# Kernel optimization log

Measured on AMD Instinct MI355X. Metric: run time of the kernel, lower is better.

The kernel has to match this reference:

```python
import jax, jax.numpy as jnp
import numpy as np

N = 640   # nodes
H = 64    # hidden_channels == base feature dim (required by MLP input dims)
DEG = 12  # random directed edges per node before symmetrization


def _mlp(x, Wa, ba, Wb, bb):
    # 2-layer MLP: Linear -> ReLU -> Linear (use_bn=False hardcoded in convs; dropout inactive in eval)
    return jax.nn.relu(x @ Wa + ba) @ Wb + bb


def setup_inputs() -> dict:
    key = jax.random.key(0)
    ks = jax.random.split(key, 8)
    x = jax.random.normal(ks[0], (N, H), dtype=jnp.float32)
    E0 = N * DEG
    src = jax.random.randint(ks[1], (E0,), 0, N)
    dst = jax.random.randint(ks[2], (E0,), 0, N)
    # undirected edge list (both directions), matching PyG k_hop_subgraph semantics on symmetric graphs
    edge_index = jnp.stack([jnp.concatenate([src, dst]), jnp.concatenate([dst, src])])
    batch = jnp.zeros((N,), dtype=jnp.int32)  # unused by the module's forward

    def lin(k, fin, fout):
        kw, kb = jax.random.split(k)
        bound = 1.0 / np.sqrt(fin)
        W = jax.random.uniform(kw, (fin, fout), minval=-bound, maxval=bound, dtype=jnp.float32)
        b = jax.random.uniform(kb, (fout,), minval=-bound, maxval=bound, dtype=jnp.float32)
        return W, b

    W1a, b1a = lin(ks[3], H + 2, H)      # convs[1] mlp: (H+t) -> H
    W1b, b1b = lin(ks[4], H, H + 1)      #               H -> (H+t-1)
    W0a, b0a = lin(ks[5], H + 1, H)      # convs[0] mlp: (H+1) -> H
    W0b, b0b = lin(ks[6], H, H)          #               H -> H
    return dict(x=x, W1a=W1a, b1a=b1a, W1b=W1b, b1b=b1b,
                W0a=W0a, b0a=b0a, W0b=W0b, b0b=b0b,
                edge_index=edge_index, batch=batch)


def reference(x, W1a, b1a, W1b, b1b, W0a, b0a, W0b, b0b, edge_index, batch):
    n = x.shape[0]
    # dense adjacency; self-loops have no effect in the original recursion -> zero diagonal
    A = jnp.zeros((n, n), x.dtype).at[edge_index[0], edge_index[1]].set(1.0)
    A = A * (1.0 - jnp.eye(n, dtype=x.dtype))

    # ---- level 1 (last level, r[1]=1), vectorized over all ego pairs (v, u) ----
    # S2(v,u) = nbrs(u) & S_v (common neighbors of v and u, excluding v, u)
    # sum_{w in S2} x_w  and  |S2|
    Y = A[:, :, None] * x[None, :, :]              # [v, w, d]
    T = jnp.einsum('vwd,uw->vud', Y, A)            # [v, u, d] = sum_w A[v,w] A[u,w] x_w
    cnt = A @ A.T                                  # [v, u] common-neighbor counts
    # hv_u = [x_u, 1, 0]; sum over S2 of [x_w, 1, 1]  ->  GIN input [x_u + T, 1 + cnt, cnt]
    inp1 = jnp.concatenate([x[None, :, :] + T,
                            (1.0 + cnt)[..., None],
                            cnt[..., None]], axis=-1)  # [v, u, H+2]
    out1 = _mlp(inp1, W1a, b1a, W1b, b1b)              # [v, u, H+1]

    # ---- level 0 (r[0]=1): GIN over u in S_v ----
    agg = jnp.einsum('vu,vud->vd', A, out1)            # sum of level-1 embeddings over S_v
    hv = jnp.concatenate([x, jnp.zeros((n, 1), x.dtype)], axis=-1)  # [x_v, 0]
    return _mlp(hv + agg, W0a, b0a, W0b, b0b)          # [N, H]
```

## Files before the change

kernel.cpp:

```cpp
#include <hip/hip_runtime.h>

#define NN   640
#define NW   20
#define NWP  24
#define H    64
#define MAXD 96

__global__ __launch_bounds__(512) void prep(
    const int* __restrict__ ei, int E,
    const float* __restrict__ x,
    const float* __restrict__ W1a, const float* __restrict__ W0a,
    const float* __restrict__ W1b, const float* __restrict__ b1b,
    unsigned* __restrict__ bits, float* __restrict__ xa, float* __restrict__ xc,
    float* __restrict__ Wf, float* __restrict__ bf)
{
    const int t = threadIdx.x, lane = t & 63, wave = t >> 6, bid = blockIdx.x;

    if (bid < 160) {
        __shared__ unsigned sb[4 * NW];
        if (t < 4 * NW) sb[t] = 0u;
        __syncthreads();

        const int quads = E >> 2;
        for (int k = t; k < quads; k += 512) {
            const int4 a4 = ((const int4*)ei)[k];
            if ((a4.x >> 2) == bid || (a4.y >> 2) == bid ||
                (a4.z >> 2) == bid || (a4.w >> 2) == bid) {
                const int4 b4 = ((const int4*)(ei + E))[k];
                if ((a4.x >> 2) == bid && a4.x != b4.x)
                    atomicOr(&sb[(a4.x & 3) * NW + (b4.x >> 5)], 1u << (b4.x & 31));
                if ((a4.y >> 2) == bid && a4.y != b4.y)
                    atomicOr(&sb[(a4.y & 3) * NW + (b4.y >> 5)], 1u << (b4.y & 31));
                if ((a4.z >> 2) == bid && a4.z != b4.z)
                    atomicOr(&sb[(a4.z & 3) * NW + (b4.z >> 5)], 1u << (b4.z & 31));
                if ((a4.w >> 2) == bid && a4.w != b4.w)
                    atomicOr(&sb[(a4.w & 3) * NW + (b4.w >> 5)], 1u << (b4.w & 31));
            }
        }
        for (int k = (quads << 2) + t; k < E; k += 512) {
            const int a = ei[k], b = ei[k + E];
            if ((a >> 2) == bid && a != b)
                atomicOr(&sb[(a & 3) * NW + (b >> 5)], 1u << (b & 31));
        }

        const int v = bid * 4 + (wave >> 1);
        const float* W = (wave & 1) ? W0a : W1a;
        const float xv = x[v * H + lane];
        float a0 = 0, a1 = 0, a2 = 0, a3 = 0;
        #pragma unroll
        for (int k = 0; k < H; k += 4) {
            a0 += __shfl(xv, k, 64)     * W[k * H + lane];
            a1 += __shfl(xv, k + 1, 64) * W[(k + 1) * H + lane];
            a2 += __shfl(xv, k + 2, 64) * W[(k + 2) * H + lane];
            a3 += __shfl(xv, k + 3, 64) * W[(k + 3) * H + lane];
        }
        float r = (a0 + a1) + (a2 + a3);
        if (wave & 1) xc[v * H + lane] = r; else xa[v * H + lane] = r;

        __syncthreads();
        if (t < 4 * NW) bits[(bid * 4 + t / NW) * NWP + (t % NW)] = sb[t];
    } else if (bid < 168) {
        const int d = (bid - 160) * 8 + wave;
        const float wv = W1b[d * 65 + lane];
        float a0 = 0, a1 = 0, a2 = 0, a3 = 0;
        #pragma unroll
        for (int e = 0; e < 64; e += 4) {
            a0 += __shfl(wv, e, 64)     * W0a[e * H + lane];
            a1 += __shfl(wv, e + 1, 64) * W0a[(e + 1) * H + lane];
            a2 += __shfl(wv, e + 2, 64) * W0a[(e + 2) * H + lane];
            a3 += __shfl(wv, e + 3, 64) * W0a[(e + 3) * H + lane];
        }
        Wf[d * H + lane] = (a0 + a1) + (a2 + a3) + W1b[d * 65 + 64] * W0a[64 * H + lane];
    } else if (wave == 0) {
        const float bv = b1b[lane];
        float a0 = 0, a1 = 0, a2 = 0, a3 = 0;
        #pragma unroll
        for (int e = 0; e < 64; e += 4) {
            a0 += __shfl(bv, e, 64)     * W0a[e * H + lane];
            a1 += __shfl(bv, e + 1, 64) * W0a[(e + 1) * H + lane];
            a2 += __shfl(bv, e + 2, 64) * W0a[(e + 2) * H + lane];
            a3 += __shfl(bv, e + 3, 64) * W0a[(e + 3) * H + lane];
        }
        bf[lane] = (a0 + a1) + (a2 + a3) + b1b[64] * W0a[64 * H + lane];
    }
}

__global__ __launch_bounds__(512, 6) void fused(
    const float* __restrict__ xa,  const float* __restrict__ xc,
    const float* __restrict__ W1a, const float* __restrict__ b1a,
    const float* __restrict__ Wf,  const float* __restrict__ bf,
    const float* __restrict__ b0a,
    const float* __restrict__ W0b, const float* __restrict__ b0b,
    const unsigned* __restrict__ bits,
    float* __restrict__ out)
{
    __shared__ __align__(16) unsigned rowv[NW];
    __shared__ __align__(16) unsigned nbs[MAXD * NW];
    __shared__ float xr[MAXD][H];
    __shared__ float p1[8][H];
    __shared__ float p2[8][H];
    __shared__ unsigned short ulist[MAXD];
    __shared__ int pre[NW];
    __shared__ int s_deg;

    const int v = blockIdx.x, t = threadIdx.x;
    const int lane = t & 63, wave = t >> 6;

    if (t < NW) rowv[t] = bits[v * NWP + t];
    __syncthreads();

    if (wave == 0) {
        unsigned word = (lane < NW) ? rowv[lane] : 0u;
        int pc = __popc(word), scan = pc;
        #pragma unroll
        for (int off = 1; off < 32; off <<= 1) {
            int nb = __shfl_up(scan, off, 64);
            if (lane >= off) scan += nb;
        }
        int o = scan - pc;
        if (lane < NW) pre[lane] = o;
        unsigned c = word;
        while (c) {
            int b = __ffs(c) - 1; c &= c - 1;
            if (o < MAXD) ulist[o] = (unsigned short)(lane * 32 + b);
            ++o;
        }
        if (lane == NW - 1) s_deg = (o < MAXD) ? o : MAXD;
    }
    __syncthreads();
    const int deg = s_deg;

    for (int p = wave; p < deg; p += 8)
        xr[p][lane] = xa[ulist[p] * H + lane];
    for (int idx = t; idx < deg * NW; idx += 512) {
        const int p = idx / NW, w = idx - p * NW;
        nbs[p * NW + w] = bits[ulist[p] * NWP + w];
    }

    const float r64 = W1a[64 * H + lane];
    const float k0  = b1a[lane] + r64;
    const float k1  = r64 + W1a[65 * H + lane];

    unsigned rw[NW];
    #pragma unroll
    for (int j = 0; j < NW; ++j) rw[j] = rowv[j];
    __syncthreads();

    float hacc = 0.f;
    for (int p = wave; p < deg; p += 8) {
        const uint4* bu = (const uint4*)(nbs + p * NW);
        const uint4 q0 = bu[0], q1 = bu[1], q2 = bu[2], q3 = bu[3], q4 = bu[4];
        unsigned cw[NW] = {
            rw[0]  & q0.x, rw[1]  & q0.y, rw[2]  & q0.z, rw[3]  & q0.w,
            rw[4]  & q1.x, rw[5]  & q1.y, rw[6]  & q1.z, rw[7]  & q1.w,
            rw[8]  & q2.x, rw[9]  & q2.y, rw[10] & q2.z, rw[11] & q2.w,
            rw[12] & q3.x, rw[13] & q3.y, rw[14] & q3.z, rw[15] & q3.w,
            rw[16] & q4.x, rw[17] & q4.y, rw[18] & q4.z, rw[19] & q4.w };
        int cnt = 0;
        #pragma unroll
        for (int j = 0; j < NW; ++j) cnt += __popc(cw[j]);
        float xs = 0.f;
        #pragma unroll
        for (int j = 0; j < NW; ++j) {
            unsigned c = cw[j];
            while (c) {
                int b = __ffs(c) - 1; c &= c - 1;
                int pos = pre[j] + __popc(rw[j] & ((1u << b) - 1));
                xs += xr[pos][lane];
            }
        }
        float h = xr[p][lane] + xs + k0 + (float)cnt * k1;
        hacc += fmaxf(h, 0.f);
    }
    p1[wave][lane] = hacc;
    __syncthreads();

    float hs = 0.f;
    #pragma unroll
    for (int w = 0; w < 8; ++w) hs += p1[w][lane];
    float s = 0.f;
    #pragma unroll
    for (int i = 0; i < 8; ++i) {
        const int d = wave * 8 + i;
        s += __shfl(hs, d, 64) * Wf[d * H + lane];
    }
    p2[wave][lane] = s;
    __syncthreads();

    float s2 = 0.f;
    #pragma unroll
    for (int w = 0; w < 8; ++w) s2 += p2[w][lane];
    const float hh = fmaxf(xc[v * H + lane] + (float)deg * bf[lane]
                           + b0a[lane] + s2, 0.f);
    float o = 0.f;
    #pragma unroll
    for (int i = 0; i < 8; ++i) {
        const int d = wave * 8 + i;
        o += __shfl(hh, d, 64) * W0b[d * H + lane];
    }
    p1[wave][lane] = o;
    __syncthreads();
    if (wave == 0) {
        float oo = b0b[lane];
        #pragma unroll
        for (int w = 0; w < 8; ++w) oo += p1[w][lane];
        out[v * H + lane] = oo;
    }
}

extern "C" void kernel_launch(void* const* d_in, const int* in_sizes, int n_in,
                              void* d_out, int out_size, void* d_ws, size_t ws_size,
                              hipStream_t stream) {
    const float* x   = (const float*)d_in[0];
    const float* W1a = (const float*)d_in[1];
    const float* b1a = (const float*)d_in[2];
    const float* W1b = (const float*)d_in[3];
    const float* b1b = (const float*)d_in[4];
    const float* W0a = (const float*)d_in[5];
    const float* b0a = (const float*)d_in[6];
    const float* W0b = (const float*)d_in[7];
    const float* b0b = (const float*)d_in[8];
    const int*   ei  = (const int*)d_in[9];
    const int    E   = in_sizes[9] / 2;

    char* ws = (char*)d_ws;
    unsigned* bits = (unsigned*)(ws);
    float*    xa   = (float*)(ws + 61440);
    float*    xc   = (float*)(ws + 61440 + 163840);
    float*    Wf   = (float*)(ws + 61440 + 2 * 163840);
    float*    bf   = (float*)(ws + 61440 + 2 * 163840 + 16384);

    prep<<<169, 512, 0, stream>>>(ei, E, x, W1a, W0a, W1b, b1b, bits, xa, xc, Wf, bf);
    fused<<<NN, 512, 0, stream>>>(xa, xc, W1a, b1a, Wf, bf, b0a, W0b, b0b,
                                  bits, (float*)d_out);
}
```

Baseline: 20.77 us.

## Compute neighbor list per wave in registers and batch edge loads in prep

In the fused kernel, each wave now reads the row bitmask straight into registers, computes prefix counts and walks the neighbor bits itself. Each wave gathers only the neighbor rows whose position maps to it. This removes the shared-memory ulist/pre/deg stage and two block-wide barriers, at the cost of every wave repeating the scalar bit walk. In prep, the edge-list scan preloads up to 8 int4 pairs per thread before doing the atomics, which gives more memory-level parallelism. It drops the early filter that skipped loading destinations, so more bytes are read.

New measurement: 23.95 us. 1.15x slower.

```diff
diff --git a/kernel.cpp b/kernel.cpp
--- a/kernel.cpp
+++ b/kernel.cpp
@@ -22,20 +22,40 @@
         __syncthreads();
 
         const int quads = E >> 2;
-        for (int k = t; k < quads; k += 512) {
+        int4 A[8], B[8];
+        #pragma unroll
+        for (int i = 0; i < 8; ++i) {
+            const int k = t + (i << 9);
+            if (k < quads) {
+                A[i] = ((const int4*)ei)[k];
+                B[i] = ((const int4*)(ei + E))[k];
+            }
+        }
+        #pragma unroll
+        for (int i = 0; i < 8; ++i) {
+            const int k = t + (i << 9);
+            if (k < quads) {
+                if ((A[i].x >> 2) == bid && A[i].x != B[i].x)
+                    atomicOr(&sb[(A[i].x & 3) * NW + (B[i].x >> 5)], 1u << (B[i].x & 31));
+                if ((A[i].y >> 2) == bid && A[i].y != B[i].y)
+                    atomicOr(&sb[(A[i].y & 3) * NW + (B[i].y >> 5)], 1u << (B[i].y & 31));
+                if ((A[i].z >> 2) == bid && A[i].z != B[i].z)
+                    atomicOr(&sb[(A[i].z & 3) * NW + (B[i].z >> 5)], 1u << (B[i].z & 31));
+                if ((A[i].w >> 2) == bid && A[i].w != B[i].w)
+                    atomicOr(&sb[(A[i].w & 3) * NW + (B[i].w >> 5)], 1u << (B[i].w & 31));
+            }
+        }
+        for (int k = t + (8 << 9); k < quads; k += 512) {
             const int4 a4 = ((const int4*)ei)[k];
-            if ((a4.x >> 2) == bid || (a4.y >> 2) == bid ||
-                (a4.z >> 2) == bid || (a4.w >> 2) == bid) {
-                const int4 b4 = ((const int4*)(ei + E))[k];
-                if ((a4.x >> 2) == bid && a4.x != b4.x)
-                    atomicOr(&sb[(a4.x & 3) * NW + (b4.x >> 5)], 1u << (b4.x & 31));
-                if ((a4.y >> 2) == bid && a4.y != b4.y)
-                    atomicOr(&sb[(a4.y & 3) * NW + (b4.y >> 5)], 1u << (b4.y & 31));
-                if ((a4.z >> 2) == bid && a4.z != b4.z)
-                    atomicOr(&sb[(a4.z & 3) * NW + (b4.z >> 5)], 1u << (b4.z & 31));
-                if ((a4.w >> 2) == bid && a4.w != b4.w)
-                    atomicOr(&sb[(a4.w & 3) * NW + (b4.w >> 5)], 1u << (b4.w & 31));
-            }
+            const int4 b4 = ((const int4*)(ei + E))[k];
+            if ((a4.x >> 2) == bid && a4.x != b4.x)
+                atomicOr(&sb[(a4.x & 3) * NW + (b4.x >> 5)], 1u << (b4.x & 31));
+            if ((a4.y >> 2) == bid && a4.y != b4.y)
+                atomicOr(&sb[(a4.y & 3) * NW + (b4.y >> 5)], 1u << (b4.y & 31));
+            if ((a4.z >> 2) == bid && a4.z != b4.z)
+                atomicOr(&sb[(a4.z & 3) * NW + (b4.z >> 5)], 1u << (b4.z & 31));
+            if ((a4.w >> 2) == bid && a4.w != b4.w)
+                atomicOr(&sb[(a4.w & 3) * NW + (b4.w >> 5)], 1u << (b4.w & 31));
         }
         for (int k = (quads << 2) + t; k < E; k += 512) {
             const int a = ei[k], b = ei[k + E];
@@ -94,56 +114,44 @@
     const unsigned* __restrict__ bits,
     float* __restrict__ out)
 {
-    __shared__ __align__(16) unsigned rowv[NW];
     __shared__ __align__(16) unsigned nbs[MAXD * NW];
     __shared__ float xr[MAXD][H];
     __shared__ float p1[8][H];
     __shared__ float p2[8][H];
-    __shared__ unsigned short ulist[MAXD];
-    __shared__ int pre[NW];
-    __shared__ int s_deg;
 
     const int v = blockIdx.x, t = threadIdx.x;
     const int lane = t & 63, wave = t >> 6;
 
-    if (t < NW) rowv[t] = bits[v * NWP + t];
-    __syncthreads();
-
-    if (wave == 0) {
-        unsigned word = (lane < NW) ? rowv[lane] : 0u;
-        int pc = __popc(word), scan = pc;
-        #pragma unroll
-        for (int off = 1; off < 32; off <<= 1) {
-            int nb = __shfl_up(scan, off, 64);
-            if (lane >= off) scan += nb;
-        }
-        int o = scan - pc;
-        if (lane < NW) pre[lane] = o;
-        unsigned c = word;
+    const uint4* bp = (const uint4*)(bits + v * NWP);
+    const uint4 R0 = bp[0], R1 = bp[1], R2 = bp[2], R3 = bp[3], R4 = bp[4];
+    const unsigned rw[NW] = { R0.x, R0.y, R0.z, R0.w, R1.x, R1.y, R1.z, R1.w,
+                              R2.x, R2.y, R2.z, R2.w, R3.x, R3.y, R3.z, R3.w,
+                              R4.x, R4.y, R4.z, R4.w };
+    int pre[NW];
+    int pos = 0;
+    #pragma unroll
+    for (int j = 0; j < NW; ++j) { pre[j] = pos; pos += __popc(rw[j]); }
+    const int deg = (pos < MAXD) ? pos : MAXD;
+
+    pos = 0;
+    #pragma unroll
+    for (int j = 0; j < NW; ++j) {
+        unsigned c = rw[j];
         while (c) {
-            int b = __ffs(c) - 1; c &= c - 1;
-            if (o < MAXD) ulist[o] = (unsigned short)(lane * 32 + b);
-            ++o;
-        }
-        if (lane == NW - 1) s_deg = (o < MAXD) ? o : MAXD;
-    }
-    __syncthreads();
-    const int deg = s_deg;
-
-    for (int p = wave; p < deg; p += 8)
-        xr[p][lane] = xa[ulist[p] * H + lane];
-    for (int idx = t; idx < deg * NW; idx += 512) {
-        const int p = idx / NW, w = idx - p * NW;
-        nbs[p * NW + w] = bits[ulist[p] * NWP + w];
+            const int b = __ffs(c) - 1; c &= c - 1;
+            if (pos < MAXD && (pos & 7) == wave) {
+                const int u = j * 32 + b;
+                xr[pos][lane] = xa[u * H + lane];
+                if (lane < 5)
+                    ((uint4*)nbs)[pos * 5 + lane] = ((const uint4*)(bits + u * NWP))[lane];
+            }
+            ++pos;
+        }
     }
 
     const float r64 = W1a[64 * H + lane];
     const float k0  = b1a[lane] + r64;
     const float k1  = r64 + W1a[65 * H + lane];
-
-    unsigned rw[NW];
-    #pragma unroll
-    for (int j = 0; j < NW; ++j) rw[j] = rowv[j];
     __syncthreads();
 
     float hacc = 0.f;
@@ -165,8 +173,8 @@
             unsigned c = cw[j];
             while (c) {
                 int b = __ffs(c) - 1; c &= c - 1;
-                int pos = pre[j] + __popc(rw[j] & ((1u << b) - 1));
-                xs += xr[pos][lane];
+                int ps = pre[j] + __popc(rw[j] & ((1u << b) - 1));
+                xs += xr[ps][lane];
             }
         }
         float h = xr[p][lane] + xs + k0 + (float)cnt * k1;
```

## Batch edge loads in prep and precompute neighbor lists for the fused kernel

Applied to the files above, without the earlier changes.

The edge-scan loop in prep now issues up to eight int4 loads of both source and destination arrays before processing, which raises memory-level parallelism in exchange for more registers. The 4-node blocks in prep also build each node's sorted neighbor list and degree and write them to workspace. The fused kernel then loads them directly instead of serially extracting bits in wave 0, which removes one barrier and the serial ffs loop from every block's critical path. The cost is extra global writes and reads for the lists and unconditional loads of the destination array.

New measurement: 20.47 us, median of 2. Within noise of the previous version (-1.5%).

```diff
diff --git a/kernel.cpp b/kernel.cpp
--- a/kernel.cpp
+++ b/kernel.cpp
@@ -12,7 +12,8 @@
     const float* __restrict__ W1a, const float* __restrict__ W0a,
     const float* __restrict__ W1b, const float* __restrict__ b1b,
     unsigned* __restrict__ bits, float* __restrict__ xa, float* __restrict__ xc,
-    float* __restrict__ Wf, float* __restrict__ bf)
+    float* __restrict__ Wf, float* __restrict__ bf,
+    unsigned short* __restrict__ ulg, int* __restrict__ degg)
 {
     const int t = threadIdx.x, lane = t & 63, wave = t >> 6, bid = blockIdx.x;
 
@@ -22,20 +23,40 @@
         __syncthreads();
 
         const int quads = E >> 2;
-        for (int k = t; k < quads; k += 512) {
+        int4 A[8], B[8];
+        #pragma unroll
+        for (int i = 0; i < 8; ++i) {
+            const int k = t + (i << 9);
+            if (k < quads) {
+                A[i] = ((const int4*)ei)[k];
+                B[i] = ((const int4*)(ei + E))[k];
+            }
+        }
+        #pragma unroll
+        for (int i = 0; i < 8; ++i) {
+            const int k = t + (i << 9);
+            if (k < quads) {
+                if ((A[i].x >> 2) == bid && A[i].x != B[i].x)
+                    atomicOr(&sb[(A[i].x & 3) * NW + (B[i].x >> 5)], 1u << (B[i].x & 31));
+                if ((A[i].y >> 2) == bid && A[i].y != B[i].y)
+                    atomicOr(&sb[(A[i].y & 3) * NW + (B[i].y >> 5)], 1u << (B[i].y & 31));
+                if ((A[i].z >> 2) == bid && A[i].z != B[i].z)
+                    atomicOr(&sb[(A[i].z & 3) * NW + (B[i].z >> 5)], 1u << (B[i].z & 31));
+                if ((A[i].w >> 2) == bid && A[i].w != B[i].w)
+                    atomicOr(&sb[(A[i].w & 3) * NW + (B[i].w >> 5)], 1u << (B[i].w & 31));
+            }
+        }
+        for (int k = t + (8 << 9); k < quads; k += 512) {
             const int4 a4 = ((const int4*)ei)[k];
-            if ((a4.x >> 2) == bid || (a4.y >> 2) == bid ||
-                (a4.z >> 2) == bid || (a4.w >> 2) == bid) {
-                const int4 b4 = ((const int4*)(ei + E))[k];
-                if ((a4.x >> 2) == bid && a4.x != b4.x)
-                    atomicOr(&sb[(a4.x & 3) * NW + (b4.x >> 5)], 1u << (b4.x & 31));
-                if ((a4.y >> 2) == bid && a4.y != b4.y)
-                    atomicOr(&sb[(a4.y & 3) * NW + (b4.y >> 5)], 1u << (b4.y & 31));
-                if ((a4.z >> 2) == bid && a4.z != b4.z)
-                    atomicOr(&sb[(a4.z & 3) * NW + (b4.z >> 5)], 1u << (b4.z & 31));
-                if ((a4.w >> 2) == bid && a4.w != b4.w)
-                    atomicOr(&sb[(a4.w & 3) * NW + (b4.w >> 5)], 1u << (b4.w & 31));
-            }
+            const int4 b4 = ((const int4*)(ei + E))[k];
+            if ((a4.x >> 2) == bid && a4.x != b4.x)
+                atomicOr(&sb[(a4.x & 3) * NW + (b4.x >> 5)], 1u << (b4.x & 31));
+            if ((a4.y >> 2) == bid && a4.y != b4.y)
+                atomicOr(&sb[(a4.y & 3) * NW + (b4.y >> 5)], 1u << (b4.y & 31));
+            if ((a4.z >> 2) == bid && a4.z != b4.z)
+                atomicOr(&sb[(a4.z & 3) * NW + (b4.z >> 5)], 1u << (b4.z & 31));
+            if ((a4.w >> 2) == bid && a4.w != b4.w)
+                atomicOr(&sb[(a4.w & 3) * NW + (b4.w >> 5)], 1u << (b4.w & 31));
         }
         for (int k = (quads << 2) + t; k < E; k += 512) {
             const int a = ei[k], b = ei[k + E];
@@ -59,6 +80,26 @@
 
         __syncthreads();
         if (t < 4 * NW) bits[(bid * 4 + t / NW) * NWP + (t % NW)] = sb[t];
+
+        if (wave < 4) {
+            const int n = bid * 4 + wave;
+            const unsigned word = (lane < NW) ? sb[wave * NW + lane] : 0u;
+            const int pc = __popc(word);
+            int scan = pc;
+            #pragma unroll
+            for (int off = 1; off < 32; off <<= 1) {
+                int nb = __shfl_up(scan, off, 64);
+                if (lane >= off) scan += nb;
+            }
+            int o = scan - pc;
+            unsigned c = word;
+            while (c) {
+                const int b = __ffs(c) - 1; c &= c - 1;
+                if (o < MAXD) ulg[n * MAXD + o] = (unsigned short)(lane * 32 + b);
+                ++o;
+            }
+            if (lane == NW - 1) degg[n] = (o < MAXD) ? o : MAXD;
+        }
     } else if (bid < 168) {
         const int d = (bid - 160) * 8 + wave;
         const float wv = W1b[d * 65 + lane];
@@ -92,14 +133,15 @@
     const float* __restrict__ b0a,
     const float* __restrict__ W0b, const float* __restrict__ b0b,
     const unsigned* __restrict__ bits,
+    const unsigned short* __restrict__ ulg, const int* __restrict__ degg,
     float* __restrict__ out)
 {
     __shared__ __align__(16) unsigned rowv[NW];
     __shared__ __align__(16) unsigned nbs[MAXD * NW];
+    __shared__ __align__(4) unsigned short ulist[MAXD];
     __shared__ float xr[MAXD][H];
     __shared__ float p1[8][H];
     __shared__ float p2[8][H];
-    __shared__ unsigned short ulist[MAXD];
     __shared__ int pre[NW];
     __shared__ int s_deg;
 
@@ -107,7 +149,11 @@
     const int lane = t & 63, wave = t >> 6;
 
     if (t < NW) rowv[t] = bits[v * NWP + t];
-    __syncthreads();
+    if (t >= 64 && t < 64 + MAXD / 2)
+        ((unsigned*)ulist)[t - 64] = ((const unsigned*)(ulg + v * MAXD))[t - 64];
+    if (t == 32) s_deg = degg[v];
+    __syncthreads();
+    const int deg = s_deg;
 
     if (wave == 0) {
         unsigned word = (lane < NW) ? rowv[lane] : 0u;
@@ -117,19 +163,8 @@
             int nb = __shfl_up(scan, off, 64);
             if (lane >= off) scan += nb;
         }
-        int o = scan - pc;
-        if (lane < NW) pre[lane] = o;
-        unsigned c = word;
-        while (c) {
-            int b = __ffs(c) - 1; c &= c - 1;
-            if (o < MAXD) ulist[o] = (unsigned short)(lane * 32 + b);
-            ++o;
-        }
-        if (lane == NW - 1) s_deg = (o < MAXD) ? o : MAXD;
-    }
-    __syncthreads();
-    const int deg = s_deg;
-
+        if (lane < NW) pre[lane] = scan - pc;
+    }
     for (int p = wave; p < deg; p += 8)
         xr[p][lane] = xa[ulist[p] * H + lane];
     for (int idx = t; idx < deg * NW; idx += 512) {
@@ -165,8 +200,8 @@
             unsigned c = cw[j];
             while (c) {
                 int b = __ffs(c) - 1; c &= c - 1;
-                int pos = pre[j] + __popc(rw[j] & ((1u << b) - 1));
-                xs += xr[pos][lane];
+                int ps = pre[j] + __popc(rw[j] & ((1u << b) - 1));
+                xs += xr[ps][lane];
             }
         }
         float h = xr[p][lane] + xs + k0 + (float)cnt * k1;
@@ -224,13 +259,16 @@
     const int    E   = in_sizes[9] / 2;
 
     char* ws = (char*)d_ws;
-    unsigned* bits = (unsigned*)(ws);
-    float*    xa   = (float*)(ws + 61440);
-    float*    xc   = (float*)(ws + 61440 + 163840);
-    float*    Wf   = (float*)(ws + 61440 + 2 * 163840);
-    float*    bf   = (float*)(ws + 61440 + 2 * 163840 + 16384);
-
-    prep<<<169, 512, 0, stream>>>(ei, E, x, W1a, W0a, W1b, b1b, bits, xa, xc, Wf, bf);
+    unsigned*       bits = (unsigned*)(ws);
+    float*          xa   = (float*)(ws + 61440);
+    float*          xc   = (float*)(ws + 61440 + 163840);
+    float*          Wf   = (float*)(ws + 389120);
+    float*          bf   = (float*)(ws + 405504);
+    unsigned short* ulg  = (unsigned short*)(ws + 405888);
+    int*            degg = (int*)(ws + 528768);
+
+    prep<<<169, 512, 0, stream>>>(ei, E, x, W1a, W0a, W1b, b1b,
+                                  bits, xa, xc, Wf, bf, ulg, degg);
     fused<<<NN, 512, 0, stream>>>(xa, xc, W1a, b1a, Wf, bf, b0a, W0b, b0b,
-                                  bits, (float*)d_out);
+                                  bits, ulg, degg, (float*)d_out);
 }
```
